# Kernel optimization log

Hardware: AMD Instinct MI355X
Metric: run time of the kernel (lower is better)

The kernel has to match this reference:

```python
import jax, jax.numpy as jnp
import numpy as np

T, B, F, H, O = 512, 64, 128, 512, 16


def setup_inputs() -> dict:
    key = jax.random.key(0)
    ks = jax.random.split(key, 8)
    s = 1.0 / np.sqrt(H)  # torch RNN/Linear default uniform init scale
    u = lambda k, shape: jax.random.uniform(k, shape, jnp.float32, -s, s)
    return {
        "x_rnn": jax.random.normal(ks[0], (T, B, F), jnp.float32),
        "w_ih": u(ks[1], (3 * H, F)),   # gate order: r, z, n (PyTorch GRU)
        "w_hh": u(ks[2], (3 * H, H)),
        "b_ih": u(ks[3], (3 * H,)),
        "b_hh": u(ks[4], (3 * H,)),
        "w_out": u(ks[5], (O, H)),
        "b_out": u(ks[6], (O,)),
    }


def reference(x_rnn, w_ih, w_hh, b_ih, b_hh, w_out, b_out):
    # Single-layer GRU, seq-first (T, B, F), h0 = zeros (torch default when hx=None).
    h_dim = w_hh.shape[1]
    # Precompute all input-side gate pre-activations in one big GEMM: (T, B, 3H)
    xg = jnp.einsum("tbf,gf->tbg", x_rnn, w_ih) + b_ih

    def step(h, xg_t):
        hg = h @ w_hh.T + b_hh               # (B, 3H)
        xr, xz, xn = jnp.split(xg_t, 3, axis=-1)
        hr, hz, hn = jnp.split(hg, 3, axis=-1)
        r = jax.nn.sigmoid(xr + hr)
        z = jax.nn.sigmoid(xz + hz)
        n = jnp.tanh(xn + r * hn)
        h_new = (1.0 - z) * n + z * h
        return h_new, h_new

    h0 = jnp.zeros((x_rnn.shape[1], h_dim), x_rnn.dtype)
    _, hs = jax.lax.scan(step, h0, xg)       # hs: (T, B, H)
    # Output projection y = hs @ W_out^T + b_out -> (T, B, O)
    return jnp.einsum("tbh,oh->tbo", hs, w_out) + b_out
```

## Files before the change

kernel.cpp:

```cpp
#include <hip/hip_runtime.h>
#include <stdint.h>
#include <stddef.h>


#define T_LEN 512
#define B_SZ  64
#define F_DIM 128
#define H_DIM 512
#define O_DIM 16
#define SENTINEL 0xAAAAAAAAu

typedef __attribute__((ext_vector_type(8))) short short8;
typedef __attribute__((ext_vector_type(4))) float floatx4;
typedef __attribute__((ext_vector_type(4))) unsigned int uintx4;

#define MFMA16(a, b, c) __builtin_amdgcn_mfma_f32_16x16x32_bf16((a), (b), (c), 0, 0, 0)

__device__ __forceinline__ unsigned short f2bf(float f) {
  unsigned u = __builtin_bit_cast(unsigned, f);
  u += 0x7fffu + ((u >> 16) & 1u);
  return (unsigned short)(u >> 16);
}

__device__ __forceinline__ float fastrcp(float d) {
  float r = __builtin_amdgcn_rcpf(d);
  return r * (2.0f - d * r);
}

__device__ __forceinline__ float sigmoidf_(float x) {
  return fastrcp(1.0f + __expf(-x));
}

__device__ __forceinline__ float tanhf_(float x) {
  float v = fminf(fmaxf(x, -10.f), 10.f);
  float e = __expf(2.f * v);
  return (e - 1.f) * fastrcp(e + 1.f);
}

__device__ __forceinline__ short8 cvt8(floatx4 f0, floatx4 f1) {
  short8 a;
  a[0] = (short)f2bf(f0[0]); a[1] = (short)f2bf(f0[1]);
  a[2] = (short)f2bf(f0[2]); a[3] = (short)f2bf(f0[3]);
  a[4] = (short)f2bf(f1[0]); a[5] = (short)f2bf(f1[1]);
  a[6] = (short)f2bf(f1[2]); a[7] = (short)f2bf(f1[3]);
  return a;
}

__device__ __forceinline__ void hissue4(floatx4* hf, const unsigned short* hbase) {
  asm volatile(
      "global_load_dwordx4 %0, %4, off sc1\n\t"
      "global_load_dwordx4 %1, %4, off offset:64 sc1\n\t"
      "global_load_dwordx4 %2, %4, off offset:128 sc1\n\t"
      "global_load_dwordx4 %3, %4, off offset:192 sc1"
      : "=&v"(hf[0]), "=&v"(hf[1]), "=&v"(hf[2]), "=&v"(hf[3])
      : "v"(hbase)
      : "memory");
}

__device__ __forceinline__ void hload4_sc1(floatx4* hf, const unsigned short* hbase) {
  asm volatile(
      "global_load_dwordx4 %0, %4, off sc1\n\t"
      "global_load_dwordx4 %1, %4, off offset:64 sc1\n\t"
      "global_load_dwordx4 %2, %4, off offset:128 sc1\n\t"
      "global_load_dwordx4 %3, %4, off offset:192 sc1\n\t"
      "s_waitcnt vmcnt(0)"
      : "=&v"(hf[0]), "=&v"(hf[1]), "=&v"(hf[2]), "=&v"(hf[3])
      : "v"(hbase)
      : "memory");
}

__device__ __forceinline__ bool clean4(const floatx4* hf) {
  bool ok = true;
  #pragma unroll
  for (int i = 0; i < 4; ++i) {
    uintx4 u = __builtin_bit_cast(uintx4, hf[i]);
    ok = ok & (u[0] != SENTINEL) & (u[1] != SENTINEL) &
         (u[2] != SENTINEL) & (u[3] != SENTINEL);
  }
  return __ballot(!ok) == 0ull;
}

__global__ __launch_bounds__(256, 1)
void gru_fused(const float* __restrict__ x,
               const float* __restrict__ w_ih,
               const float* __restrict__ w_hh,
               const float* __restrict__ b_ih,
               const float* __restrict__ b_hh,
               const float* __restrict__ w_out,
               const float* __restrict__ b_out,
               unsigned short* __restrict__ hs,
               float* __restrict__ y) {
  __shared__ __align__(16) float part[2][4][16][33][4];

  const int tid  = threadIdx.x;
  const int lane = tid & 63;
  const int wv   = tid >> 6;
  const int n16  = lane & 15;
  const int quad = lane >> 4;
  const floatx4 fzero = {0.f, 0.f, 0.f, 0.f};

  if (blockIdx.x < 64) {
    const int bg      = blockIdx.x >> 4;
    const int cg      = blockIdx.x & 15;
    const int bgbase  = bg * 16;
    const int colbase = cg * 32;

    short8 bwx[3][2];
    short8 bwh[3][2][4];
    #pragma unroll
    for (int g = 0; g < 3; ++g) {
      #pragma unroll
      for (int nt = 0; nt < 2; ++nt) {
        const int grow = g * H_DIM + colbase + nt * 16 + n16;
        const float* pih = w_ih + (size_t)grow * F_DIM + wv * 32 + quad * 8;
        {
          short8 v;
          #pragma unroll
          for (int j = 0; j < 8; ++j) v[j] = (short)f2bf(pih[j]);
          bwx[g][nt] = v;
        }
        const float* phh = w_hh + (size_t)grow * H_DIM + wv * 128 + quad * 8;
        #pragma unroll
        for (int i = 0; i < 4; ++i) {
          short8 v;
          #pragma unroll
          for (int j = 0; j < 8; ++j) v[j] = (short)f2bf(phh[i * 32 + j]);
          bwh[g][nt][i] = v;
        }
      }
    }

    const int ew_b  = tid >> 4;
    const int ew_j0 = (tid & 15) * 2;
    float b_rz[2], b_zz[2], b_in[2], b_hn[2];
    #pragma unroll
    for (int e = 0; e < 2; ++e) {
      const int c = colbase + ew_j0 + e;
      b_rz[e] = b_ih[c] + b_hh[c];
      b_zz[e] = b_ih[H_DIM + c] + b_hh[H_DIM + c];
      b_in[e] = b_ih[2 * H_DIM + c];
      b_hn[e] = b_hh[2 * H_DIM + c];
    }
    float hm[2] = {0.0f, 0.0f};

    floatx4 xf0, xf1;
    {
      const float* px = x + ((size_t)(bgbase + n16)) * F_DIM + wv * 32 + quad * 8;
      xf0 = *(const floatx4*)px;
      xf1 = *(const floatx4*)(px + 4);
    }
    short8 a_x = cvt8(xf0, xf1);

    floatx4 aR0, aR1, aZ0, aZ1, aX0, aX1, aH0, aH1;
    floatx4 hf[4] = {fzero, fzero, fzero, fzero};
    int mguard = 1 << 18;

    auto epilogue = [&](int t) {
      const int tb = t & 1;
      #pragma unroll
      for (int i = 0; i < 4; ++i) {
        const int r = quad * 4 + i;
        floatx4 v0 = {aR0[i], aZ0[i], aX0[i], aH0[i]};
        floatx4 v1 = {aR1[i], aZ1[i], aX1[i], aH1[i]};
        *(floatx4*)&part[tb][wv][r][n16][0]      = v0;
        *(floatx4*)&part[tb][wv][r][16 + n16][0] = v1;
      }
      __syncthreads();
      if (t + 1 < T_LEN) a_x = cvt8(xf0, xf1);
      float pr[2] = {0.f, 0.f}, pz[2] = {0.f, 0.f};
      float pn[2] = {0.f, 0.f}, ph[2] = {0.f, 0.f};
      #pragma unroll
      for (int w = 0; w < 4; ++w) {
        #pragma unroll
        for (int e = 0; e < 2; ++e) {
          floatx4 g = *(const floatx4*)&part[tb][w][ew_b][ew_j0 + e][0];
          pr[e] += g[0]; pz[e] += g[1]; pn[e] += g[2]; ph[e] += g[3];
        }
      }
      unsigned short hb2[2];
      #pragma unroll
      for (int e = 0; e < 2; ++e) {
        const float r = sigmoidf_(pr[e] + b_rz[e]);
        const float z = sigmoidf_(pz[e] + b_zz[e]);
        const float n = tanhf_(pn[e] + b_in[e] + r * (ph[e] + b_hn[e]));
        const float hn2 = (1.0f - z) * n + z * hm[e];
        hm[e] = hn2;
        hb2[e] = f2bf(hn2);
      }
      const unsigned int packed = ((unsigned int)hb2[1] << 16) | (unsigned int)hb2[0];
      unsigned int* dst = (unsigned int*)(hs +
          ((size_t)(t * B_SZ + bgbase + ew_b)) * H_DIM + colbase + ew_j0);
      asm volatile("global_atomic_swap %0, %1, off sc1"
                   :: "v"(dst), "v"(packed) : "memory");
    };

    {
      aR0 = MFMA16(a_x, bwx[0][0], fzero); aR1 = MFMA16(a_x, bwx[0][1], fzero);
      aZ0 = MFMA16(a_x, bwx[1][0], fzero); aZ1 = MFMA16(a_x, bwx[1][1], fzero);
      aX0 = MFMA16(a_x, bwx[2][0], fzero); aX1 = MFMA16(a_x, bwx[2][1], fzero);
      aH0 = fzero; aH1 = fzero;
      {
        const float* pxn = x + ((size_t)(B_SZ + bgbase + n16)) * F_DIM + wv * 32 + quad * 8;
        asm volatile("global_load_dwordx4 %0, %2, off\n\t"
                     "global_load_dwordx4 %1, %2, off offset:16"
                     : "=&v"(xf0), "=&v"(xf1) : "v"(pxn) : "memory");
      }
      asm volatile("s_waitcnt vmcnt(0)" ::: "memory");
      __builtin_amdgcn_sched_barrier(0);
      epilogue(0);
    }

    for (int t = 1; t < T_LEN; ++t) {
      aR0 = MFMA16(a_x, bwx[0][0], fzero); aR1 = MFMA16(a_x, bwx[0][1], fzero);
      aZ0 = MFMA16(a_x, bwx[1][0], fzero); aZ1 = MFMA16(a_x, bwx[1][1], fzero);
      aX0 = MFMA16(a_x, bwx[2][0], fzero); aX1 = MFMA16(a_x, bwx[2][1], fzero);
      aH0 = fzero; aH1 = fzero;
      __builtin_amdgcn_sched_barrier(0);

      const unsigned short* hbase =
          hs + ((size_t)((t - 1) * B_SZ + bgbase + n16)) * H_DIM + wv * 128 + quad * 8;
      while (true) {
        hload4_sc1(hf, hbase);
        if (clean4(hf)) break;
        if (--mguard <= 0) break;
      }

      if (t + 1 < T_LEN) {
        const float* pxn = x + ((size_t)((t + 1) * B_SZ + bgbase + n16)) * F_DIM +
                           wv * 32 + quad * 8;
        asm volatile("global_load_dwordx4 %0, %2, off\n\t"
                     "global_load_dwordx4 %1, %2, off offset:16"
                     : "=&v"(xf0), "=&v"(xf1) : "v"(pxn) : "memory");
      }

      #pragma unroll
      for (int i = 0; i < 4; ++i) {
        short8 a = __builtin_bit_cast(short8, hf[i]);
        aR0 = MFMA16(a, bwh[0][0][i], aR0); aR1 = MFMA16(a, bwh[0][1][i], aR1);
        aZ0 = MFMA16(a, bwh[1][0][i], aZ0); aZ1 = MFMA16(a, bwh[1][1][i], aZ1);
        aH0 = MFMA16(a, bwh[2][0][i], aH0); aH1 = MFMA16(a, bwh[2][1][i], aH1);
      }

      __builtin_amdgcn_sched_barrier(0);
      asm volatile("s_waitcnt vmcnt(0)" ::: "memory");
      __builtin_amdgcn_sched_barrier(0);

      epilogue(t);
    }
  } else {
    const int p = (int)blockIdx.x - 64;

    short8 bw[16];
    const float* pw = w_out + (size_t)n16 * H_DIM + quad * 8;
    #pragma unroll
    for (int kc = 0; kc < 16; ++kc) {
      short8 v;
      #pragma unroll
      for (int j = 0; j < 8; ++j) v[j] = (short)f2bf(pw[kc * 32 + j]);
      bw[kc] = v;
    }
    const float bo = b_out[n16];

    int sguard = 1 << 12;
    int fguard = 1 << 10;

    for (int k = 0; k < 8; ++k) {
      const int t = p * 8 + k;
      const size_t rowb = (size_t)t * B_SZ + wv * 16;

      {
        const int srow = lane & 15;
        const int scg  = ((lane >> 4) * 4 + (srow & 3)) & 15;
        const unsigned short* sp = hs + (rowb + srow) * H_DIM + scg * 32 + 12;
        while (true) {
          unsigned int sv;
          asm volatile("global_load_dword %0, %1, off sc1\n\t"
                       "s_waitcnt vmcnt(0)"
                       : "=&v"(sv) : "v"(sp) : "memory");
          __builtin_amdgcn_sched_barrier(0);
          if (__ballot(sv == SENTINEL) == 0ull) break;
          if (--sguard <= 0) break;
          __builtin_amdgcn_s_sleep(48);
        }
      }

      floatx4 hv[16];
      const unsigned short* hb = hs + (rowb + n16) * H_DIM + quad * 8;
      while (true) {
        #pragma unroll
        for (int g = 0; g < 4; ++g) hissue4(&hv[4 * g], hb + g * 128);
        asm volatile("s_waitcnt vmcnt(0)" ::: "memory");
        __builtin_amdgcn_sched_barrier(0);
        bool ok = true;
        #pragma unroll
        for (int i = 0; i < 16; ++i) {
          uintx4 u = __builtin_bit_cast(uintx4, hv[i]);
          ok = ok & (u[0] != SENTINEL) & (u[1] != SENTINEL) &
               (u[2] != SENTINEL) & (u[3] != SENTINEL);
        }
        if (__ballot(!ok) == 0ull) break;
        if (--fguard <= 0) break;
        __builtin_amdgcn_s_sleep(8);
      }

      floatx4 acc = fzero;
      #pragma unroll
      for (int kc = 0; kc < 16; ++kc)
        acc = MFMA16(__builtin_bit_cast(short8, hv[kc]), bw[kc], acc);
      #pragma unroll
      for (int i = 0; i < 4; ++i) {
        const size_t r = rowb + quad * 4 + i;
        y[r * O_DIM + n16] = acc[i] + bo;
      }
    }
  }
}

extern "C" void kernel_launch(void* const* d_in, const int* in_sizes, int n_in,
                              void* d_out, int out_size, void* d_ws, size_t ws_size,
                              hipStream_t stream) {
  (void)in_sizes; (void)n_in; (void)out_size; (void)ws_size;
  const float* x     = (const float*)d_in[0];
  const float* w_ih  = (const float*)d_in[1];
  const float* w_hh  = (const float*)d_in[2];
  const float* b_ih  = (const float*)d_in[3];
  const float* b_hh  = (const float*)d_in[4];
  const float* w_out = (const float*)d_in[5];
  const float* b_out = (const float*)d_in[6];
  float* y = (float*)d_out;

  unsigned short* hs = (unsigned short*)d_ws;

  gru_fused<<<128, 256, 0, stream>>>(x, w_ih, w_hh, b_ih, b_hh, w_out, b_out, hs, y);
}
```

Baseline: 1.300 ms.

## Interleave GRU and projection blocks, try sc0 polling loads, use atomic store

```diff
diff --git a/kernel.cpp b/kernel.cpp
--- a/kernel.cpp
+++ b/kernel.cpp
@@ -63,6 +63,18 @@
       "global_load_dwordx4 %1, %4, off offset:64 sc1\n\t"
       "global_load_dwordx4 %2, %4, off offset:128 sc1\n\t"
       "global_load_dwordx4 %3, %4, off offset:192 sc1\n\t"
+      "s_waitcnt vmcnt(0)"
+      : "=&v"(hf[0]), "=&v"(hf[1]), "=&v"(hf[2]), "=&v"(hf[3])
+      : "v"(hbase)
+      : "memory");
+}
+
+__device__ __forceinline__ void hload4_sc0(floatx4* hf, const unsigned short* hbase) {
+  asm volatile(
+      "global_load_dwordx4 %0, %4, off sc0\n\t"
+      "global_load_dwordx4 %1, %4, off offset:64 sc0\n\t"
+      "global_load_dwordx4 %2, %4, off offset:128 sc0\n\t"
+      "global_load_dwordx4 %3, %4, off offset:192 sc0\n\t"
       "s_waitcnt vmcnt(0)"
       : "=&v"(hf[0]), "=&v"(hf[1]), "=&v"(hf[2]), "=&v"(hf[3])
       : "v"(hbase)
@@ -99,9 +111,11 @@
   const int quad = lane >> 4;
   const floatx4 fzero = {0.f, 0.f, 0.f, 0.f};
 
-  if (blockIdx.x < 64) {
-    const int bg      = blockIdx.x >> 4;
-    const int cg      = blockIdx.x & 15;
+  const int slot = (int)blockIdx.x & 7;
+
+  if (slot < 4) {
+    const int bg      = slot;
+    const int cg      = (int)blockIdx.x >> 3;
     const int bgbase  = bg * 16;
     const int colbase = cg * 32;
 
@@ -149,11 +163,12 @@
       xf0 = *(const floatx4*)px;
       xf1 = *(const floatx4*)(px + 4);
     }
-    short8 a_x = cvt8(xf0, xf1);
 
     floatx4 aR0, aR1, aZ0, aZ1, aX0, aX1, aH0, aH1;
     floatx4 hf[4] = {fzero, fzero, fzero, fzero};
-    int mguard = 1 << 18;
+    int mguard  = 1 << 18;
+    int use_sc0 = 1;
+    int s0wins  = 0;
 
     auto epilogue = [&](int t) {
       const int tb = t & 1;
@@ -166,7 +181,6 @@
         *(floatx4*)&part[tb][wv][r][16 + n16][0] = v1;
       }
       __syncthreads();
-      if (t + 1 < T_LEN) a_x = cvt8(xf0, xf1);
       float pr[2] = {0.f, 0.f}, pz[2] = {0.f, 0.f};
       float pn[2] = {0.f, 0.f}, ph[2] = {0.f, 0.f};
       #pragma unroll
@@ -190,47 +204,49 @@
       const unsigned int packed = ((unsigned int)hb2[1] << 16) | (unsigned int)hb2[0];
       unsigned int* dst = (unsigned int*)(hs +
           ((size_t)(t * B_SZ + bgbase + ew_b)) * H_DIM + colbase + ew_j0);
-      asm volatile("global_atomic_swap %0, %1, off sc1"
-                   :: "v"(dst), "v"(packed) : "memory");
+      __hip_atomic_store(dst, packed, __ATOMIC_RELAXED, __HIP_MEMORY_SCOPE_AGENT);
     };
 
     {
+      short8 a = cvt8(xf0, xf1);
+      aR0 = MFMA16(a, bwx[0][0], fzero); aR1 = MFMA16(a, bwx[0][1], fzero);
+      aZ0 = MFMA16(a, bwx[1][0], fzero); aZ1 = MFMA16(a, bwx[1][1], fzero);
+      aX0 = MFMA16(a, bwx[2][0], fzero); aX1 = MFMA16(a, bwx[2][1], fzero);
+      aH0 = fzero; aH1 = fzero;
+      const float* px = x + ((size_t)(B_SZ + bgbase + n16)) * F_DIM + wv * 32 + quad * 8;
+      xf0 = *(const floatx4*)px;
+      xf1 = *(const floatx4*)(px + 4);
+      epilogue(0);
+    }
+
+    for (int t = 1; t < T_LEN; ++t) {
+      short8 a_x = cvt8(xf0, xf1);
       aR0 = MFMA16(a_x, bwx[0][0], fzero); aR1 = MFMA16(a_x, bwx[0][1], fzero);
       aZ0 = MFMA16(a_x, bwx[1][0], fzero); aZ1 = MFMA16(a_x, bwx[1][1], fzero);
       aX0 = MFMA16(a_x, bwx[2][0], fzero); aX1 = MFMA16(a_x, bwx[2][1], fzero);
       aH0 = fzero; aH1 = fzero;
-      {
-        const float* pxn = x + ((size_t)(B_SZ + bgbase + n16)) * F_DIM + wv * 32 + quad * 8;
-        asm volatile("global_load_dwordx4 %0, %2, off\n\t"
-                     "global_load_dwordx4 %1, %2, off offset:16"
-                     : "=&v"(xf0), "=&v"(xf1) : "v"(pxn) : "memory");
-      }
-      asm volatile("s_waitcnt vmcnt(0)" ::: "memory");
-      __builtin_amdgcn_sched_barrier(0);
-      epilogue(0);
-    }
-
-    for (int t = 1; t < T_LEN; ++t) {
-      aR0 = MFMA16(a_x, bwx[0][0], fzero); aR1 = MFMA16(a_x, bwx[0][1], fzero);
-      aZ0 = MFMA16(a_x, bwx[1][0], fzero); aZ1 = MFMA16(a_x, bwx[1][1], fzero);
-      aX0 = MFMA16(a_x, bwx[2][0], fzero); aX1 = MFMA16(a_x, bwx[2][1], fzero);
-      aH0 = fzero; aH1 = fzero;
-      __builtin_amdgcn_sched_barrier(0);
 
       const unsigned short* hbase =
           hs + ((size_t)((t - 1) * B_SZ + bgbase + n16)) * H_DIM + wv * 128 + quad * 8;
-      while (true) {
-        hload4_sc1(hf, hbase);
-        if (clean4(hf)) break;
-        if (--mguard <= 0) break;
+      {
+        int tries = use_sc0 ? 3 : 0;
+        bool won0 = false;
+        while (true) {
+          const bool via0 = (tries > 0);
+          if (via0) { hload4_sc0(hf, hbase); --tries; }
+          else      { hload4_sc1(hf, hbase); }
+          if (clean4(hf)) { won0 = via0; break; }
+          if (--mguard <= 0) break;
+        }
+        s0wins += (int)won0;
+        if (t == 8 && s0wins == 0) use_sc0 = 0;
       }
 
       if (t + 1 < T_LEN) {
-        const float* pxn = x + ((size_t)((t + 1) * B_SZ + bgbase + n16)) * F_DIM +
-                           wv * 32 + quad * 8;
-        asm volatile("global_load_dwordx4 %0, %2, off\n\t"
-                     "global_load_dwordx4 %1, %2, off offset:16"
-                     : "=&v"(xf0), "=&v"(xf1) : "v"(pxn) : "memory");
+        const float* px = x + ((size_t)((t + 1) * B_SZ + bgbase + n16)) * F_DIM +
+                          wv * 32 + quad * 8;
+        xf0 = *(const floatx4*)px;
+        xf1 = *(const floatx4*)(px + 4);
       }
 
       #pragma unroll
@@ -241,14 +257,10 @@
         aH0 = MFMA16(a, bwh[2][0][i], aH0); aH1 = MFMA16(a, bwh[2][1][i], aH1);
       }
 
-      __builtin_amdgcn_sched_barrier(0);
-      asm volatile("s_waitcnt vmcnt(0)" ::: "memory");
-      __builtin_amdgcn_sched_barrier(0);
-
       epilogue(t);
     }
   } else {
-    const int p = (int)blockIdx.x - 64;
+    const int p = (((int)blockIdx.x >> 3) << 2) | (slot - 4);
 
     short8 bw[16];
     const float* pw = w_out + (size_t)n16 * H_DIM + quad * 8;
```

Measured after the change: 1.725 ms. 1.33x slower.
